# Optimization experiments

Hardware: AMD Instinct MI355X
Metric: run time of the kernel (lower is better)

## Reference

```python
import jax, jax.numpy as jnp
import numpy as np

EMBED_DIM = 256
NUM_HEADS = 4
HEAD_DIM = EMBED_DIM // NUM_HEADS
SCALE = HEAD_DIM ** (-0.5)


def setup_inputs() -> dict:
    key = jax.random.key(0)
    kx, kq, kp, kb = jax.random.split(key, 4)
    B, N, C = 4, 4096, EMBED_DIM
    x = jax.random.normal(kx, (B, N, C), dtype=jnp.float32)
    # qkv: Linear(C, 3C, bias=False); torch stores weight as [out, in]
    w_qkv = jax.random.normal(kq, (3 * C, C), dtype=jnp.float32) * (C ** -0.5)
    w_proj = jax.random.normal(kp, (C, C), dtype=jnp.float32) * (C ** -0.5)
    b_proj = jax.random.normal(kb, (C,), dtype=jnp.float32) * 0.01
    return {"x": x, "w_qkv": w_qkv, "w_proj": w_proj, "b_proj": b_proj}


def reference(x, w_qkv, w_proj, b_proj):
    B, N, C = x.shape
    H, D = NUM_HEADS, HEAD_DIM
    # qkv projection: [B,N,3C] -> [3,B,H,N,D]
    qkv = (x @ w_qkv.T).reshape(B, N, 3, H, D).transpose(2, 0, 3, 1, 4)
    q, k, v = qkv[0], qkv[1], qkv[2]
    # materialized [B,H,N,N] scores (faithful to the original)
    attn = jnp.einsum("bhnd,bhmd->bhnm", q, k) * SCALE
    attn_probs = jax.nn.softmax(attn, axis=-1)
    out = jnp.einsum("bhnm,bhmd->bhnd", attn_probs, v)
    out = out.transpose(0, 2, 1, 3).reshape(B, N, C)
    return out @ w_proj.T + b_proj
```

## Files before the change

kernel.cpp:

```cpp
#include <hip/hip_runtime.h>
#include <hip/hip_bf16.h>

typedef __hip_bfloat16 bf16;
typedef _Float16 f16;
typedef __attribute__((ext_vector_type(8))) short bf16x8;
typedef __attribute__((ext_vector_type(8))) _Float16 f16x8;
typedef __attribute__((ext_vector_type(2))) _Float16 f16x2;
typedef __attribute__((ext_vector_type(4))) float f32x4;
typedef __attribute__((ext_vector_type(4))) unsigned int u32x4;
typedef __attribute__((ext_vector_type(2))) unsigned int u32x2;

#define B_ 4
#define N_ 4096
#define C_ 256
#define H_ 4
#define D_ 64
#define KLN 0.18033688011112042f

#if __has_builtin(__builtin_amdgcn_exp2f)
#define EXP2(x) __builtin_amdgcn_exp2f(x)
#else
#define EXP2(x) exp2f(x)
#endif
#if __has_builtin(__builtin_amdgcn_rcpf)
#define RCP(x) __builtin_amdgcn_rcpf(x)
#else
#define RCP(x) (1.0f / (x))
#endif

__device__ inline unsigned int pk2(float a, float b) {
    unsigned int ua = __builtin_bit_cast(unsigned int, a) + 0x8000u;
    unsigned int ub = __builtin_bit_cast(unsigned int, b) + 0x8000u;
    return (ua >> 16) | (ub & 0xffff0000u);
}
__device__ inline unsigned int pkh2(float a, float b) {
#if __has_builtin(__builtin_amdgcn_cvt_pkrtz)
    return __builtin_bit_cast(unsigned int, __builtin_amdgcn_cvt_pkrtz(a, b));
#else
    f16x2 h = { (f16)a, (f16)b };
    return __builtin_bit_cast(unsigned int, h);
#endif
}
__device__ inline short f2s(float x) {
    return (short)__builtin_bit_cast(unsigned short, __float2bfloat16(x));
}
__device__ inline bf16x8 cvt8(const float* __restrict__ p) {
    f32x4 a = *reinterpret_cast<const f32x4*>(p);
    f32x4 b = *reinterpret_cast<const f32x4*>(p + 4);
    bf16x8 r = { f2s(a[0]), f2s(a[1]), f2s(a[2]), f2s(a[3]),
                 f2s(b[0]), f2s(b[1]), f2s(b[2]), f2s(b[3]) };
    return r;
}

__global__ __launch_bounds__(256) void cast_bf16(const float* __restrict__ x,
                                                 const float* __restrict__ wq,
                                                 const float* __restrict__ wp,
                                                 bf16* __restrict__ xb,
                                                 bf16* __restrict__ wqb,
                                                 bf16* __restrict__ wpb)
{
    int bid = blockIdx.x;
    const float* s; bf16* d; int base;
    if (bid < 2048)      { s = x;  d = xb;  base = bid * 2048; }
    else if (bid < 2144) { s = wq; d = wqb; base = (bid - 2048) * 2048; }
    else                 { s = wp; d = wpb; base = (bid - 2144) * 2048; }
    int i = base + threadIdx.x * 8;
    f32x4 a = *reinterpret_cast<const f32x4*>(s + i);
    f32x4 b = *reinterpret_cast<const f32x4*>(s + i + 4);
    u32x4 o;
    o.x = pk2(a[0], a[1]); o.y = pk2(a[2], a[3]);
    o.z = pk2(b[0], b[1]); o.w = pk2(b[2], b[3]);
    *reinterpret_cast<u32x4*>(d + i) = o;
}

__global__ __launch_bounds__(256, 2) void qkv_fast(const bf16* __restrict__ x,
                                                   const bf16* __restrict__ w,
                                                   bf16* __restrict__ qw,
                                                   bf16* __restrict__ kw,
                                                   f16* __restrict__ vtw)
{
    __shared__ short w_s[64][264];
    const int tid  = threadIdx.x;
    const int lane = tid & 63;
    const int wav  = tid >> 6;
    const int quad = lane >> 4;
    const int l16  = lane & 15;
    const int mt = blockIdx.x / 12, nb = blockIdx.x % 12;
    const int m0 = mt * 64, n0 = nb * 64;

    {
        const int row = tid >> 2, cb = (tid & 3) * 64;
        const bf16* src = w + (size_t)(n0 + row) * C_ + cb;
#pragma unroll
        for (int i = 0; i < 8; ++i)
            *reinterpret_cast<bf16x8*>(&w_s[row][cb + i * 8]) =
                *reinterpret_cast<const bf16x8*>(src + i * 8);
    }
    __syncthreads();

    f32x4 acc[4] = {{0,0,0,0},{0,0,0,0},{0,0,0,0},{0,0,0,0}};
    const bf16* xrow = x + (size_t)(m0 + wav * 16 + l16) * C_ + quad * 8;
#pragma unroll
    for (int k0 = 0; k0 < C_; k0 += 32) {
        bf16x8 a = *reinterpret_cast<const bf16x8*>(xrow + k0);
#pragma unroll
        for (int nt = 0; nt < 4; ++nt) {
            bf16x8 b = *reinterpret_cast<const bf16x8*>(&w_s[nt * 16 + l16][k0 + quad * 8]);
            acc[nt] = __builtin_amdgcn_mfma_f32_16x16x32_bf16(a, b, acc[nt], 0, 0, 0);
        }
    }

    const int bb = m0 >> 12;
    const int nbase = (m0 + wav * 16) & (N_ - 1);
    if (nb < 4) {
        const int h = nb;
#pragma unroll
        for (int nt = 0; nt < 4; ++nt)
#pragma unroll
            for (int r = 0; r < 4; ++r) {
                int n = nbase + quad * 4 + r, d = nt * 16 + l16;
                qw[(((size_t)bb * H_ + h) * N_ + n) * D_ + d] =
                    __float2bfloat16(acc[nt][r] * KLN);
            }
    } else if (nb < 8) {
        const int h = nb - 4;
#pragma unroll
        for (int nt = 0; nt < 4; ++nt)
#pragma unroll
            for (int r = 0; r < 4; ++r) {
                int n = nbase + quad * 4 + r, d = nt * 16 + l16;
                kw[(((size_t)bb * H_ + h) * N_ + n) * D_ + d] =
                    __float2bfloat16(acc[nt][r]);
            }
    } else {
        const int h = nb - 8;
#pragma unroll
        for (int nt = 0; nt < 4; ++nt) {
            int d = nt * 16 + l16;
            u32x2 wv;
            wv.x = pkh2(acc[nt][0], acc[nt][1]);
            wv.y = pkh2(acc[nt][2], acc[nt][3]);
            *reinterpret_cast<u32x2*>(
                vtw + (((size_t)bb * H_ + h) * D_ + d) * N_ + nbase + quad * 4) = wv;
        }
    }
}

__global__ __launch_bounds__(256) void qkv_cvt(const float* __restrict__ x,
                                               const float* __restrict__ w,
                                               bf16* __restrict__ qw,
                                               bf16* __restrict__ kw,
                                               f16* __restrict__ vtw)
{
    const int lane = threadIdx.x & 63;
    const int wav  = threadIdx.x >> 6;
    const int quad = lane >> 4;
    const int l16  = lane & 15;
    const int gw   = blockIdx.x * 4 + wav;
    const int m0   = (gw / 12) * 16;
    const int n0   = (gw % 12) * 64;

    f32x4 acc[4] = {{0,0,0,0},{0,0,0,0},{0,0,0,0},{0,0,0,0}};
    const float* xrow = x + (size_t)(m0 + l16) * C_ + quad * 8;
#pragma unroll
    for (int k0 = 0; k0 < C_; k0 += 32) {
        bf16x8 a = cvt8(xrow + k0);
#pragma unroll
        for (int nt = 0; nt < 4; ++nt) {
            bf16x8 b = cvt8(w + (size_t)(n0 + nt * 16 + l16) * C_ + k0 + quad * 8);
            acc[nt] = __builtin_amdgcn_mfma_f32_16x16x32_bf16(a, b, acc[nt], 0, 0, 0);
        }
    }
#pragma unroll
    for (int nt = 0; nt < 4; ++nt)
#pragma unroll
        for (int r = 0; r < 4; ++r) {
            int m  = m0 + quad * 4 + r;
            int o  = n0 + nt * 16 + l16;
            int bb = m >> 12;
            int n  = m & (N_ - 1);
            if (o < 256) {
                int h = o >> 6, d = o & 63;
                qw[(((size_t)bb * H_ + h) * N_ + n) * D_ + d] =
                    __float2bfloat16(acc[nt][r] * KLN);
            } else if (o < 512) {
                int oo = o - 256; int h = oo >> 6, d = oo & 63;
                kw[(((size_t)bb * H_ + h) * N_ + n) * D_ + d] =
                    __float2bfloat16(acc[nt][r]);
            } else {
                int oo = o - 512; int h = oo >> 6, d = oo & 63;
                vtw[(((size_t)bb * H_ + h) * D_ + d) * N_ + n] = (f16)acc[nt][r];
            }
        }
}

__global__ __launch_bounds__(256, 2) void attn(const bf16* __restrict__ q,
                                               const bf16* __restrict__ k,
                                               const f16* __restrict__ vt,
                                               bf16* __restrict__ o)
{
    __shared__ short        k_s[64][72];
    __shared__ f16          v_s[64][72];
    __shared__ unsigned int p_s[4][32][36];

    const int tid  = threadIdx.x;
    const int lane = tid & 63;
    const int wav  = tid >> 6;
    const int quad = lane >> 4;
    const int l16  = lane & 15;
    const int bh = blockIdx.x >> 5;
    const int qt = blockIdx.x & 31;
    const int bb = bh >> 2, h = bh & 3;

    const bf16* qp = q  + (size_t)bh * N_ * D_;
    const bf16* kp = k  + (size_t)bh * N_ * D_;
    const f16*  vp = vt + (size_t)bh * D_ * N_;

    const int qbase = qt * 128 + wav * 32;
    bf16x8 qb[2][2];
#pragma unroll
    for (int qg = 0; qg < 2; ++qg)
#pragma unroll
        for (int ks = 0; ks < 2; ++ks)
            qb[qg][ks] = *reinterpret_cast<const bf16x8*>(
                qp + (size_t)(qbase + qg * 16 + l16) * D_ + ks * 32 + quad * 8);

    const int kr0 = tid >> 3, kc0 = (tid & 7) * 8;
    const int kr1 = kr0 + 32;

    bf16x8 kst0, kst1; f16x8 vst0, vst1;
    kst0 = *reinterpret_cast<const bf16x8*>(kp + (size_t)kr0 * D_ + kc0);
    kst1 = *reinterpret_cast<const bf16x8*>(kp + (size_t)kr1 * D_ + kc0);
    vst0 = *reinterpret_cast<const f16x8*>(vp + (size_t)kr0 * N_ + kc0);
    vst1 = *reinterpret_cast<const f16x8*>(vp + (size_t)kr1 * N_ + kc0);

    f32x4 oacc[2][4] = {{{0,0,0,0},{0,0,0,0},{0,0,0,0},{0,0,0,0}},
                        {{0,0,0,0},{0,0,0,0},{0,0,0,0},{0,0,0,0}}};
    f32x4 lacc[2] = {{0,0,0,0},{0,0,0,0}};
    const f16x8 onesA = {1.f16, 1.f16, 1.f16, 1.f16, 1.f16, 1.f16, 1.f16, 1.f16};

    for (int t = 0; t < 64; ++t) {
        __syncthreads();
        *reinterpret_cast<bf16x8*>(&k_s[kr0][kc0]) = kst0;
        *reinterpret_cast<bf16x8*>(&k_s[kr1][kc0]) = kst1;
        *reinterpret_cast<f16x8*>(&v_s[kr0][kc0]) = vst0;
        *reinterpret_cast<f16x8*>(&v_s[kr1][kc0]) = vst1;
        __syncthreads();
        if (t < 63) {
            const int j0n = (t + 1) * 64;
            kst0 = *reinterpret_cast<const bf16x8*>(kp + (size_t)(j0n + kr0) * D_ + kc0);
            kst1 = *reinterpret_cast<const bf16x8*>(kp + (size_t)(j0n + kr1) * D_ + kc0);
            vst0 = *reinterpret_cast<const f16x8*>(vp + (size_t)kr0 * N_ + j0n + kc0);
            vst1 = *reinterpret_cast<const f16x8*>(vp + (size_t)kr1 * N_ + j0n + kc0);
        }

        f32x4 st[2][4] = {{{0,0,0,0},{0,0,0,0},{0,0,0,0},{0,0,0,0}},
                          {{0,0,0,0},{0,0,0,0},{0,0,0,0},{0,0,0,0}}};
#pragma unroll
        for (int nt = 0; nt < 4; ++nt) {
            bf16x8 ka0 = *reinterpret_cast<const bf16x8*>(&k_s[nt * 16 + l16][quad * 8]);
            bf16x8 ka1 = *reinterpret_cast<const bf16x8*>(&k_s[nt * 16 + l16][32 + quad * 8]);
#pragma unroll
            for (int qg = 0; qg < 2; ++qg) {
                st[qg][nt] = __builtin_amdgcn_mfma_f32_16x16x32_bf16(ka0, qb[qg][0], st[qg][nt], 0, 0, 0);
                st[qg][nt] = __builtin_amdgcn_mfma_f32_16x16x32_bf16(ka1, qb[qg][1], st[qg][nt], 0, 0, 0);
            }
        }

#pragma unroll
        for (int qg = 0; qg < 2; ++qg)
#pragma unroll
            for (int nt = 0; nt < 4; ++nt) {
                float p0 = EXP2(st[qg][nt][0]);
                float p1 = EXP2(st[qg][nt][1]);
                float p2 = EXP2(st[qg][nt][2]);
                float p3 = EXP2(st[qg][nt][3]);
                p_s[wav][qg * 16 + l16][nt * 8 + quad * 2 + 0] = pkh2(p0, p1);
                p_s[wav][qg * 16 + l16][nt * 8 + quad * 2 + 1] = pkh2(p2, p3);
            }
        asm volatile("" ::: "memory");

#pragma unroll
        for (int ks = 0; ks < 2; ++ks) {
            f16x8 pb[2];
#pragma unroll
            for (int qg = 0; qg < 2; ++qg) {
                u32x4 pw = *reinterpret_cast<const u32x4*>(
                    &p_s[wav][qg * 16 + l16][ks * 16 + quad * 4]);
                pb[qg] = __builtin_bit_cast(f16x8, pw);
                lacc[qg] = __builtin_amdgcn_mfma_f32_16x16x32_f16(onesA, pb[qg], lacc[qg], 0, 0, 0);
            }
#pragma unroll
            for (int dt = 0; dt < 4; ++dt) {
                f16x8 va = *reinterpret_cast<const f16x8*>(&v_s[dt * 16 + l16][ks * 32 + quad * 8]);
#pragma unroll
                for (int qg = 0; qg < 2; ++qg)
                    oacc[qg][dt] = __builtin_amdgcn_mfma_f32_16x16x32_f16(va, pb[qg], oacc[qg][dt], 0, 0, 0);
            }
        }
    }

#pragma unroll
    for (int qg = 0; qg < 2; ++qg) {
        float rl = RCP(lacc[qg][0]);
        const size_t obase = ((size_t)bb * N_ + qbase + qg * 16 + l16) * C_ + h * D_;
#pragma unroll
        for (int dt = 0; dt < 4; ++dt) {
            u32x2 wv;
            wv.x = pk2(oacc[qg][dt][0] * rl, oacc[qg][dt][1] * rl);
            wv.y = pk2(oacc[qg][dt][2] * rl, oacc[qg][dt][3] * rl);
            *reinterpret_cast<u32x2*>(o + obase + dt * 16 + quad * 4) = wv;
        }
    }
}

__global__ __launch_bounds__(256, 2) void out_proj_fast(const bf16* __restrict__ ov,
                                                        const bf16* __restrict__ w,
                                                        const float* __restrict__ bias,
                                                        float* __restrict__ out)
{
    __shared__ short w_s[64][264];
    const int tid  = threadIdx.x;
    const int lane = tid & 63;
    const int wav  = tid >> 6;
    const int quad = lane >> 4;
    const int l16  = lane & 15;
    const int m0 = (blockIdx.x >> 2) * 64;
    const int n0 = (blockIdx.x & 3) * 64;

    {
        const int row = tid >> 2, cb = (tid & 3) * 64;
        const bf16* src = w + (size_t)(n0 + row) * C_ + cb;
#pragma unroll
        for (int i = 0; i < 8; ++i)
            *reinterpret_cast<bf16x8*>(&w_s[row][cb + i * 8]) =
                *reinterpret_cast<const bf16x8*>(src + i * 8);
    }
    __syncthreads();

    f32x4 acc[4] = {{0,0,0,0},{0,0,0,0},{0,0,0,0},{0,0,0,0}};
    const bf16* orow = ov + (size_t)(m0 + wav * 16 + l16) * C_ + quad * 8;
#pragma unroll
    for (int k0 = 0; k0 < C_; k0 += 32) {
        bf16x8 a = *reinterpret_cast<const bf16x8*>(orow + k0);
#pragma unroll
        for (int nt = 0; nt < 4; ++nt) {
            bf16x8 b = *reinterpret_cast<const bf16x8*>(&w_s[nt * 16 + l16][k0 + quad * 8]);
            acc[nt] = __builtin_amdgcn_mfma_f32_16x16x32_bf16(a, b, acc[nt], 0, 0, 0);
        }
    }
#pragma unroll
    for (int nt = 0; nt < 4; ++nt)
#pragma unroll
        for (int r = 0; r < 4; ++r) {
            int m  = m0 + wav * 16 + quad * 4 + r;
            int oc = n0 + nt * 16 + l16;
            out[(size_t)m * C_ + oc] = acc[nt][r] + bias[oc];
        }
}

__global__ __launch_bounds__(256) void out_proj_cvt(const bf16* __restrict__ ov,
                                                    const float* __restrict__ w,
                                                    const float* __restrict__ bias,
                                                    float* __restrict__ out)
{
    const int lane = threadIdx.x & 63;
    const int wav  = threadIdx.x >> 6;
    const int quad = lane >> 4;
    const int l16  = lane & 15;
    const int gw   = blockIdx.x * 4 + wav;
    const int m0   = (gw >> 2) * 16;
    const int n0   = (gw & 3) * 64;

    f32x4 acc[4] = {{0,0,0,0},{0,0,0,0},{0,0,0,0},{0,0,0,0}};
    const bf16* orow = ov + (size_t)(m0 + l16) * C_ + quad * 8;
#pragma unroll
    for (int k0 = 0; k0 < C_; k0 += 32) {
        bf16x8 a = *reinterpret_cast<const bf16x8*>(orow + k0);
#pragma unroll
        for (int nt = 0; nt < 4; ++nt) {
            bf16x8 b = cvt8(w + (size_t)(n0 + nt * 16 + l16) * C_ + k0 + quad * 8);
            acc[nt] = __builtin_amdgcn_mfma_f32_16x16x32_bf16(a, b, acc[nt], 0, 0, 0);
        }
    }
#pragma unroll
    for (int nt = 0; nt < 4; ++nt)
#pragma unroll
        for (int r = 0; r < 4; ++r) {
            int m  = m0 + quad * 4 + r;
            int oc = n0 + nt * 16 + l16;
            out[(size_t)m * C_ + oc] = acc[nt][r] + bias[oc];
        }
}

extern "C" void kernel_launch(void* const* d_in, const int* in_sizes, int n_in,
                              void* d_out, int out_size, void* d_ws, size_t ws_size,
                              hipStream_t stream) {
    const float* x      = (const float*)d_in[0];
    const float* w_qkv  = (const float*)d_in[1];
    const float* w_proj = (const float*)d_in[2];
    const float* b_proj = (const float*)d_in[3];
    float* out = (float*)d_out;

    const size_t qkv_elems = (size_t)B_ * H_ * N_ * D_;
    bf16* q_ws  = (bf16*)d_ws;
    bf16* k_ws  = q_ws  + qkv_elems;
    f16*  vt_ws = (f16*)(k_ws + qkv_elems);
    bf16* o_ws  = (bf16*)(vt_ws + qkv_elems);
    bf16* x_bf  = o_ws  + qkv_elems;
    bf16* wq_bf = x_bf  + (size_t)B_ * N_ * C_;
    bf16* wp_bf = wq_bf + (size_t)3 * C_ * C_;

    const size_t need = ((size_t)4 * qkv_elems + (size_t)B_ * N_ * C_
                         + (size_t)3 * C_ * C_ + (size_t)C_ * C_) * 2;

    if (ws_size >= need) {
        cast_bf16    <<<2176, 256, 0, stream>>>(x, w_qkv, w_proj, x_bf, wq_bf, wp_bf);
        qkv_fast     <<<3072, 256, 0, stream>>>(x_bf, wq_bf, q_ws, k_ws, vt_ws);
        attn         <<< 512, 256, 0, stream>>>(q_ws, k_ws, vt_ws, o_ws);
        out_proj_fast<<<1024, 256, 0, stream>>>(o_ws, wp_bf, b_proj, out);
    } else {
        qkv_cvt      <<<3072, 256, 0, stream>>>(x, w_qkv, q_ws, k_ws, vt_ws);
        attn         <<< 512, 256, 0, stream>>>(q_ws, k_ws, vt_ws, o_ws);
        out_proj_cvt <<<1024, 256, 0, stream>>>(o_ws, w_proj, b_proj, out);
    }
}
```

Measured before the change: 200.5 us.

## Split attention key range across wave pairs with direct-to-LDS XOR-swizzled loads

Each wave now handles 64 query rows instead of 32, and the four waves form two pairs that each process half of the key/value sequence. The two halves' partial outputs and row sums are merged through shared memory at the end. K/V tiles are loaded straight into LDS with global_load_lds using an XOR swizzle in place of padded rows, which removes the register staging and is meant to reduce bank conflicts. The aim is more reuse of each K/V fragment per MFMA and less register traffic on loads. The cost is more accumulator registers, no prefetch overlap since the loads are issued between barriers, and an extra LDS merge step.

```diff
diff --git a/kernel.cpp b/kernel.cpp
--- a/kernel.cpp
+++ b/kernel.cpp
@@ -27,6 +27,17 @@
 #else
 #define RCP(x) (1.0f / (x))
 #endif
+
+__device__ inline void load_lds16(const void* g, void* l) {
+#if __has_builtin(__builtin_amdgcn_global_load_lds)
+    __builtin_amdgcn_global_load_lds(
+        (const __attribute__((address_space(1))) unsigned int*)g,
+        (__attribute__((address_space(3))) unsigned int*)l, 16, 0, 0);
+#else
+    int ln = __lane_id();
+    ((u32x4*)l)[ln] = *((const u32x4*)g);
+#endif
+}
 
 __device__ inline unsigned int pk2(float a, float b) {
     unsigned int ua = __builtin_bit_cast(unsigned int, a) + 0x8000u;
@@ -199,15 +210,18 @@
                                                const f16* __restrict__ vt,
                                                bf16* __restrict__ o)
 {
-    __shared__ short        k_s[64][72];
-    __shared__ f16          v_s[64][72];
-    __shared__ unsigned int p_s[4][32][36];
+    __shared__ short        k_s[2][64 * 64];
+    __shared__ f16          v_s[2][64 * 64];
+    __shared__ unsigned int p_s[4][64 * 36];
 
     const int tid  = threadIdx.x;
     const int lane = tid & 63;
     const int wav  = tid >> 6;
     const int quad = lane >> 4;
     const int l16  = lane & 15;
+    const int l8   = l16 & 7;
+    const int sub  = wav & 1;
+    const int jh   = wav >> 1;
     const int bh = blockIdx.x >> 5;
     const int qt = blockIdx.x & 31;
     const int bb = bh >> 2, h = bh & 3;
@@ -216,100 +230,118 @@
     const bf16* kp = k  + (size_t)bh * N_ * D_;
     const f16*  vp = vt + (size_t)bh * D_ * N_;
 
-    const int qbase = qt * 128 + wav * 32;
-    bf16x8 qb[2][2];
-#pragma unroll
-    for (int qg = 0; qg < 2; ++qg)
+    const int qbase = qt * 128 + sub * 64;
+    bf16x8 qb[4][2];
+#pragma unroll
+    for (int qg = 0; qg < 4; ++qg)
 #pragma unroll
         for (int ks = 0; ks < 2; ++ks)
             qb[qg][ks] = *reinterpret_cast<const bf16x8*>(
                 qp + (size_t)(qbase + qg * 16 + l16) * D_ + ks * 32 + quad * 8);
 
-    const int kr0 = tid >> 3, kc0 = (tid & 7) * 8;
-    const int kr1 = kr0 + 32;
-
-    bf16x8 kst0, kst1; f16x8 vst0, vst1;
-    kst0 = *reinterpret_cast<const bf16x8*>(kp + (size_t)kr0 * D_ + kc0);
-    kst1 = *reinterpret_cast<const bf16x8*>(kp + (size_t)kr1 * D_ + kc0);
-    vst0 = *reinterpret_cast<const f16x8*>(vp + (size_t)kr0 * N_ + kc0);
-    vst1 = *reinterpret_cast<const f16x8*>(vp + (size_t)kr1 * N_ + kc0);
-
-    f32x4 oacc[2][4] = {{{0,0,0,0},{0,0,0,0},{0,0,0,0},{0,0,0,0}},
-                        {{0,0,0,0},{0,0,0,0},{0,0,0,0},{0,0,0,0}}};
-    f32x4 lacc[2] = {{0,0,0,0},{0,0,0,0}};
+    const int ri = lane >> 3;
+    const int ci = lane & 7;
+    const int gc = ci ^ ri;
+
+    f32x4 oacc[4][4];
+    f32x4 lacc[4] = {{0,0,0,0},{0,0,0,0},{0,0,0,0},{0,0,0,0}};
+#pragma unroll
+    for (int qg = 0; qg < 4; ++qg)
+#pragma unroll
+        for (int dt = 0; dt < 4; ++dt) oacc[qg][dt] = (f32x4){0,0,0,0};
     const f16x8 onesA = {1.f16, 1.f16, 1.f16, 1.f16, 1.f16, 1.f16, 1.f16, 1.f16};
 
-    for (int t = 0; t < 64; ++t) {
+    for (int t = 0; t < 32; ++t) {
+        const int j0 = jh * 2048 + t * 64;
         __syncthreads();
-        *reinterpret_cast<bf16x8*>(&k_s[kr0][kc0]) = kst0;
-        *reinterpret_cast<bf16x8*>(&k_s[kr1][kc0]) = kst1;
-        *reinterpret_cast<f16x8*>(&v_s[kr0][kc0]) = vst0;
-        *reinterpret_cast<f16x8*>(&v_s[kr1][kc0]) = vst1;
+#pragma unroll
+        for (int g = 0; g < 4; ++g) {
+            const int rl_ = sub * 32 + g * 8;
+            load_lds16(kp + (size_t)(j0 + rl_ + ri) * D_ + gc * 8, &k_s[jh][rl_ * 64]);
+            load_lds16(vp + (size_t)(rl_ + ri) * N_ + j0 + gc * 8, &v_s[jh][rl_ * 64]);
+        }
         __syncthreads();
-        if (t < 63) {
-            const int j0n = (t + 1) * 64;
-            kst0 = *reinterpret_cast<const bf16x8*>(kp + (size_t)(j0n + kr0) * D_ + kc0);
-            kst1 = *reinterpret_cast<const bf16x8*>(kp + (size_t)(j0n + kr1) * D_ + kc0);
-            vst0 = *reinterpret_cast<const f16x8*>(vp + (size_t)kr0 * N_ + j0n + kc0);
-            vst1 = *reinterpret_cast<const f16x8*>(vp + (size_t)kr1 * N_ + j0n + kc0);
-        }
-
-        f32x4 st[2][4] = {{{0,0,0,0},{0,0,0,0},{0,0,0,0},{0,0,0,0}},
-                          {{0,0,0,0},{0,0,0,0},{0,0,0,0},{0,0,0,0}}};
-#pragma unroll
-        for (int nt = 0; nt < 4; ++nt) {
-            bf16x8 ka0 = *reinterpret_cast<const bf16x8*>(&k_s[nt * 16 + l16][quad * 8]);
-            bf16x8 ka1 = *reinterpret_cast<const bf16x8*>(&k_s[nt * 16 + l16][32 + quad * 8]);
-#pragma unroll
-            for (int qg = 0; qg < 2; ++qg) {
-                st[qg][nt] = __builtin_amdgcn_mfma_f32_16x16x32_bf16(ka0, qb[qg][0], st[qg][nt], 0, 0, 0);
-                st[qg][nt] = __builtin_amdgcn_mfma_f32_16x16x32_bf16(ka1, qb[qg][1], st[qg][nt], 0, 0, 0);
-            }
-        }
-
-#pragma unroll
-        for (int qg = 0; qg < 2; ++qg)
+
+        bf16x8 ka[4][2];
+#pragma unroll
+        for (int nt = 0; nt < 4; ++nt)
+#pragma unroll
+            for (int ks = 0; ks < 2; ++ks)
+                ka[nt][ks] = *reinterpret_cast<const bf16x8*>(
+                    &k_s[jh][(nt * 16 + l16) * 64 + (((ks << 2) + quad) ^ l8) * 8]);
+
+#pragma unroll
+        for (int qg = 0; qg < 4; ++qg) {
+            f32x4 s[4] = {{0,0,0,0},{0,0,0,0},{0,0,0,0},{0,0,0,0}};
 #pragma unroll
             for (int nt = 0; nt < 4; ++nt) {
-                float p0 = EXP2(st[qg][nt][0]);
-                float p1 = EXP2(st[qg][nt][1]);
-                float p2 = EXP2(st[qg][nt][2]);
-                float p3 = EXP2(st[qg][nt][3]);
-                p_s[wav][qg * 16 + l16][nt * 8 + quad * 2 + 0] = pkh2(p0, p1);
-                p_s[wav][qg * 16 + l16][nt * 8 + quad * 2 + 1] = pkh2(p2, p3);
-            }
+                s[nt] = __builtin_amdgcn_mfma_f32_16x16x32_bf16(ka[nt][0], qb[qg][0], s[nt], 0, 0, 0);
+                s[nt] = __builtin_amdgcn_mfma_f32_16x16x32_bf16(ka[nt][1], qb[qg][1], s[nt], 0, 0, 0);
+            }
+            unsigned int* prow = &p_s[wav][(qg * 16 + l16) * 36];
+#pragma unroll
+            for (int nt = 0; nt < 4; ++nt) {
+                float p0 = EXP2(s[nt][0]);
+                float p1 = EXP2(s[nt][1]);
+                float p2 = EXP2(s[nt][2]);
+                float p3 = EXP2(s[nt][3]);
+                u32x2 w2 = { pkh2(p0, p1), pkh2(p2, p3) };
+                *reinterpret_cast<u32x2*>(prow + nt * 8 + quad * 2) = w2;
+            }
+        }
         asm volatile("" ::: "memory");
 
 #pragma unroll
         for (int ks = 0; ks < 2; ++ks) {
-            f16x8 pb[2];
-#pragma unroll
-            for (int qg = 0; qg < 2; ++qg) {
+            f16x8 pb[4];
+#pragma unroll
+            for (int qg = 0; qg < 4; ++qg) {
                 u32x4 pw = *reinterpret_cast<const u32x4*>(
-                    &p_s[wav][qg * 16 + l16][ks * 16 + quad * 4]);
+                    &p_s[wav][(qg * 16 + l16) * 36 + ks * 16 + quad * 4]);
                 pb[qg] = __builtin_bit_cast(f16x8, pw);
                 lacc[qg] = __builtin_amdgcn_mfma_f32_16x16x32_f16(onesA, pb[qg], lacc[qg], 0, 0, 0);
             }
 #pragma unroll
             for (int dt = 0; dt < 4; ++dt) {
-                f16x8 va = *reinterpret_cast<const f16x8*>(&v_s[dt * 16 + l16][ks * 32 + quad * 8]);
-#pragma unroll
-                for (int qg = 0; qg < 2; ++qg)
+                f16x8 va = *reinterpret_cast<const f16x8*>(
+                    &v_s[jh][(dt * 16 + l16) * 64 + (((ks << 2) + quad) ^ l8) * 8]);
+#pragma unroll
+                for (int qg = 0; qg < 4; ++qg)
                     oacc[qg][dt] = __builtin_amdgcn_mfma_f32_16x16x32_f16(va, pb[qg], oacc[qg][dt], 0, 0, 0);
             }
         }
     }
 
-#pragma unroll
-    for (int qg = 0; qg < 2; ++qg) {
-        float rl = RCP(lacc[qg][0]);
-        const size_t obase = ((size_t)bb * N_ + qbase + qg * 16 + l16) * C_ + h * D_;
-#pragma unroll
-        for (int dt = 0; dt < 4; ++dt) {
-            u32x2 wv;
-            wv.x = pk2(oacc[qg][dt][0] * rl, oacc[qg][dt][1] * rl);
-            wv.y = pk2(oacc[qg][dt][2] * rl, oacc[qg][dt][3] * rl);
-            *reinterpret_cast<u32x2*>(o + obase + dt * 16 + quad * 4) = wv;
+    __syncthreads();
+    float* mrg = reinterpret_cast<float*>(p_s);
+    if (jh == 1) {
+        float* dst = mrg + (sub * 64 + lane) * 68;
+#pragma unroll
+        for (int qg = 0; qg < 4; ++qg) {
+#pragma unroll
+            for (int dt = 0; dt < 4; ++dt)
+#pragma unroll
+                for (int e = 0; e < 4; ++e)
+                    dst[qg * 17 + dt * 4 + e] = oacc[qg][dt][e];
+            dst[qg * 17 + 16] = lacc[qg][0];
+        }
+    }
+    __syncthreads();
+    if (jh == 0) {
+        const float* src = mrg + (sub * 64 + lane) * 68;
+#pragma unroll
+        for (int qg = 0; qg < 4; ++qg) {
+            float rl = RCP(lacc[qg][0] + src[qg * 17 + 16]);
+            const size_t obase = ((size_t)bb * N_ + qbase + qg * 16 + l16) * C_ + h * D_;
+#pragma unroll
+            for (int dt = 0; dt < 4; ++dt) {
+                float v0 = (oacc[qg][dt][0] + src[qg * 17 + dt * 4 + 0]) * rl;
+                float v1 = (oacc[qg][dt][1] + src[qg * 17 + dt * 4 + 1]) * rl;
+                float v2 = (oacc[qg][dt][2] + src[qg * 17 + dt * 4 + 2]) * rl;
+                float v3 = (oacc[qg][dt][3] + src[qg * 17 + dt * 4 + 3]) * rl;
+                u32x2 wv = { pk2(v0, v1), pk2(v2, v3) };
+                *reinterpret_cast<u32x2*>(o + obase + dt * 16 + quad * 4) = wv;
+            }
         }
     }
 }
```

New measurement: 186.5 us. 6.9% less time.
